# Optimization experiments

Hardware: AMD Instinct MI355X
Metric: run time of the kernel (lower is better)

Reference implementation:

```python
import jax, jax.numpy as jnp
import numpy as np

VAR_NUM = [29, 2, 1, 6, 7, 59, 1, 24, 76, 711, 3, 9, 1]  # sums to 929
TEMP = 0.8
EPS = 1e-20


def setup_inputs() -> dict:
    key = jax.random.key(0)
    ks = jax.random.split(key, 8)
    B, D, H, O = 32768, 128, 1024, 929
    s = lambda n: 1.0 / np.sqrt(n)
    return {
        "x": jax.random.normal(ks[0], (B, D), jnp.float32),
        "W1": jax.random.uniform(ks[1], (D, H), jnp.float32, -s(D), s(D)),
        "b1": jax.random.uniform(ks[2], (H,), jnp.float32, -s(D), s(D)),
        "W2": jax.random.uniform(ks[3], (H, H), jnp.float32, -s(H), s(H)),
        "b2": jax.random.uniform(ks[4], (H,), jnp.float32, -s(H), s(H)),
        "W3": jax.random.uniform(ks[5], (H, O), jnp.float32, -s(H), s(H)),
        "b3": jax.random.uniform(ks[6], (O,), jnp.float32, -s(H), s(H)),
        "u": jax.random.uniform(ks[7], (B, O), jnp.float32),  # U(0,1) gumbel base noise
    }


def reference(x, W1, b1, W2, b2, W3, b3, u):
    h = jax.nn.elu(x @ W1 + b1)          # [B, H]
    h = jax.nn.sigmoid(h @ W2 + b2)      # [B, H]
    logits = h @ W3 + b3                 # [B, 929]
    g = -jnp.log(-jnp.log(u + EPS) + EPS)  # gumbel noise, [B, 929]
    outs = []
    off = 0
    for n in VAR_NUM:  # fixed 13 segments
        seg = logits[:, off:off + n]
        if n == 1:
            outs.append(seg)  # passthrough for continuous columns
        else:
            y = (seg + g[:, off:off + n]) / TEMP
            outs.append(jax.nn.softmax(y, axis=-1))
        off += n
    return jnp.concatenate(outs, axis=1)  # [B, 929]
```

## Files before the change

### kernel.cpp

```cpp
#include <hip/hip_runtime.h>
#include <hip/hip_bf16.h>
#include <stdint.h>

#define GEPS 1e-20f

typedef __bf16 bf16x8 __attribute__((ext_vector_type(8)));
typedef float  f32x4  __attribute__((ext_vector_type(4)));

typedef const __attribute__((address_space(1))) uint32_t* gptr32;
typedef __attribute__((address_space(3))) uint32_t* lptr32;

__device__ __forceinline__ void load_lds16(const void* g, void* l) {
    __builtin_amdgcn_global_load_lds((gptr32)g, (lptr32)l, 16, 0, 0);
}

__device__ __forceinline__ uint16_t f2bf(float v) {
    __hip_bfloat16 b = __float2bfloat16(v);
    return *(uint16_t*)&b;
}
__device__ __forceinline__ float bf2f(uint16_t b) {
    uint32_t u = (uint32_t)b << 16;
    return __builtin_bit_cast(float, u);
}

#define LN2   0.69314718056f
#define LOG2E 1.44269504089f
__device__ __forceinline__ float fast_log(float x) { return __builtin_amdgcn_logf(x) * LN2; }
__device__ __forceinline__ float fast_exp(float x) { return __builtin_amdgcn_exp2f(x * LOG2E); }
__device__ __forceinline__ float fast_exp2(float x) { return __builtin_amdgcn_exp2f(x); }
__device__ __forceinline__ float fast_rcp(float x)  { return __builtin_amdgcn_rcpf(x); }

__device__ __forceinline__ void store_val(uint16_t* C, size_t idx, float v) { C[idx] = f2bf(v); }
__device__ __forceinline__ void store_val(float* C, size_t idx, float v)    { C[idx] = v; }

__global__ void cast_bf16(const float* __restrict__ in, uint16_t* __restrict__ out, int n) {
    int i = (blockIdx.x * blockDim.x + threadIdx.x) * 4;
    if (i < n) {
        float4 v = *(const float4*)(in + i);
        ushort4 o;
        o.x = f2bf(v.x); o.y = f2bf(v.y); o.z = f2bf(v.z); o.w = f2bf(v.w);
        *(ushort4*)(out + i) = o;
    }
}

__global__ void transpose_cast(const float* __restrict__ W, uint16_t* __restrict__ Wt,
                               int K, int N, int Npad) {
    __shared__ float tile[64][65];
    const int k0 = blockIdx.y * 64, n0 = blockIdx.x * 64;
    const int tx = threadIdx.x & 63, ty = threadIdx.x >> 6;
    for (int r = ty; r < 64; r += 4) {
        int n = n0 + tx;
        tile[r][tx] = (n < N) ? W[(size_t)(k0 + r) * N + n] : 0.f;
    }
    __syncthreads();
    for (int r = ty; r < 64; r += 4) {
        Wt[(size_t)(n0 + r) * K + k0 + tx] = f2bf(tile[tx][r]);
    }
}

template<int ACT, typename OutT, bool SNG>
__global__ __launch_bounds__(256)
void gemm_bt(const uint16_t* __restrict__ A, const uint16_t* __restrict__ Bt,
             const float* __restrict__ bias, OutT* __restrict__ C,
             float* __restrict__ sngl,
             int K, int Nout, int ldc) {
    __shared__ __align__(16) uint16_t As[128 * 32];
    __shared__ __align__(16) uint16_t Bs[128 * 32];

    const int t    = threadIdx.x;
    const int wave = t >> 6, lane = t & 63;

    const int nbx = gridDim.x;
    const int bid = blockIdx.y * nbx + blockIdx.x;
    const int xcd = bid & 7;
    const int s   = bid >> 3;
    const int nidx = s % nbx;
    const int midx = xcd * (gridDim.y >> 3) + s / nbx;

    const int m0 = midx * 128, n0 = nidx * 128;
    const int wm = (wave >> 1) * 64, wn = (wave & 1) * 64;
    const int quad = lane >> 4;
    const int qk   = quad * 8;
    const int r15  = lane & 15;

    f32x4 acc[4][4] = {};

    const uint16_t* Ag = A  + (size_t)m0 * K;
    const uint16_t* Bg = Bt + (size_t)n0 * K;

    for (int k0 = 0; k0 < K; k0 += 32) {
        __syncthreads();
        #pragma unroll
        for (int rd = 0; rd < 2; ++rd) {
            int c = t + rd * 256;
            int row = c >> 2, kc = (c & 3) * 8;
            load_lds16(Ag + (size_t)row * K + k0 + kc, &As[c * 8]);
            load_lds16(Bg + (size_t)row * K + k0 + kc, &Bs[c * 8]);
        }
        __syncthreads();

        bf16x8 a[4], b[4];
        #pragma unroll
        for (int i = 0; i < 4; ++i)
            a[i] = *(const bf16x8*)&As[(wm + i * 16 + r15) * 32 + qk];
        #pragma unroll
        for (int i = 0; i < 4; ++i)
            b[i] = *(const bf16x8*)&Bs[(wn + i * 16 + r15) * 32 + qk];

        #pragma unroll
        for (int mi = 0; mi < 4; ++mi)
            #pragma unroll
            for (int ni = 0; ni < 4; ++ni)
                acc[mi][ni] = __builtin_amdgcn_mfma_f32_16x16x32_bf16(
                    a[mi], b[ni], acc[mi][ni], 0, 0, 0);
    }

    #pragma unroll
    for (int ni = 0; ni < 4; ++ni) {
        int col = n0 + wn + ni * 16 + r15;
        if (col < Nout) {
            float bv = bias[col];
            bool is_sng = SNG && (col == 31 || col == 104 || col == 928);
            #pragma unroll
            for (int mi = 0; mi < 4; ++mi) {
                #pragma unroll
                for (int r = 0; r < 4; ++r) {
                    int row = m0 + wm + mi * 16 + quad * 4 + r;
                    float v = acc[mi][ni][r] + bv;
                    if (ACT == 1) v = (v > 0.f) ? v : (fast_exp(v) - 1.f);
                    else if (ACT == 2) v = fast_rcp(1.f + fast_exp(-v));
                    store_val(C, (size_t)row * ldc + col, v);
                    if constexpr (SNG) {
                        if (is_sng) sngl[(size_t)row * 929 + col] = v;
                    }
                }
            }
        }
    }
}

#define BARRIER() asm volatile("s_barrier" ::: "memory")
#define VMW6()    asm volatile("s_waitcnt vmcnt(6)" ::: "memory")
#define VMW8()    asm volatile("s_waitcnt vmcnt(8)" ::: "memory")
#define DRAIN()   asm volatile("s_waitcnt vmcnt(0) lgkmcnt(0)" ::: "memory")
#define PRIO1()   __builtin_amdgcn_s_setprio(1)
#define PRIO0()   __builtin_amdgcn_s_setprio(0)

template<int ACT, typename OutT, bool SNG, int K>
__global__ __launch_bounds__(512, 2)
void gemm256(const uint16_t* __restrict__ A, const uint16_t* __restrict__ Bt,
             const float* __restrict__ bias, OutT* __restrict__ C,
             float* __restrict__ sngl, int Nout, int ldc) {
    constexpr int NT = K / 32;
    constexpr int NI = NT / 4;
    constexpr int KB = K * 2;
    static_assert(NT >= 8 && (NT & (NT - 1)) == 0, "need pow2 >= 8 tiles");
    __shared__ __align__(16) char lds[131072];

    const int t = threadIdx.x;
    const int wave = t >> 6, lane = t & 63;
    const int quad = lane >> 4, r15 = lane & 15;
    const int wm = (wave >> 2) * 128, wn = (wave & 3) * 64;

    const int nbx = gridDim.x;
    const int bid = blockIdx.y * nbx + blockIdx.x;
    const int xcd = bid & 7;
    const int sb  = bid >> 3;
    const int nidx = sb % nbx;
    const int midx = xcd * (gridDim.y >> 3) + sb / nbx;
    const int m0 = midx * 256, n0 = nidx * 256;

    const int scb = ((t & 3) ^ ((t >> 3) & 3)) << 4;
    const char* Asrc = (const char*)A  + (size_t)(m0 + (t >> 2)) * KB + scb;
    const char* Bsrc = (const char*)Bt + (size_t)(n0 + (t >> 2)) * KB + scb;

    const int cbR   = (quad ^ ((r15 >> 1) & 3)) << 4;
    const int aRowB = (wm + r15) * 64;
    const int bRowB = (wn + r15) * 64;

    f32x4 acc[8][4] = {};
    bf16x8 aLo[4], aHi[4], bE[4], bO[4];

    auto stgA = [&](int buf, int tile) {
        const char* s = Asrc + tile * 64;
        load_lds16(s,                    &lds[buf * 32768 + t * 16]);
        load_lds16(s + (size_t)128 * KB, &lds[buf * 32768 + 8192 + t * 16]);
    };
    auto stgB = [&](int buf, int tile) {
        const char* s = Bsrc + tile * 64;
        load_lds16(s,                    &lds[buf * 32768 + 16384 + t * 16]);
        load_lds16(s + (size_t)128 * KB, &lds[buf * 32768 + 24576 + t * 16]);
    };
    auto rdAlo = [&](int buf) {
        #pragma unroll
        for (int i = 0; i < 4; ++i)
            aLo[i] = *(const bf16x8*)&lds[buf * 32768 + aRowB + i * 1024 + cbR];
    };
    auto rdAhi = [&](int buf) {
        #pragma unroll
        for (int i = 0; i < 4; ++i)
            aHi[i] = *(const bf16x8*)&lds[buf * 32768 + aRowB + (4 + i) * 1024 + cbR];
    };
    auto rdB = [&](int buf, bf16x8 (&b)[4]) {
        #pragma unroll
        for (int i = 0; i < 4; ++i)
            b[i] = *(const bf16x8*)&lds[buf * 32768 + 16384 + bRowB + i * 1024 + cbR];
    };
    auto mfma16 = [&](int mlo, bf16x8 (&a)[4], bf16x8 (&b)[4]) {
        #pragma unroll
        for (int mi = 0; mi < 4; ++mi)
            #pragma unroll
            for (int ni = 0; ni < 4; ++ni)
                acc[mlo + mi][ni] = __builtin_amdgcn_mfma_f32_16x16x32_bf16(
                    a[mi], b[ni], acc[mlo + mi][ni], 0, 0, 0);
    };

    stgA(0, 0); stgB(0, 0);
    stgA(1, 1); stgB(1, 1);
    stgA(2, 2); stgB(2, 2);
    VMW8(); BARRIER();
    rdAlo(0); rdB(0, bE);

    #pragma unroll 1
    for (int ki = 0; ki < NI; ++ki) {
        const int T = ki * 4;
        rdAhi(0); stgA(3, (T + 3) & (NT - 1));
        PRIO1(); mfma16(0, aLo, bE); PRIO0();
        VMW6(); BARRIER();
        rdAlo(1); rdB(1, bO); stgB(3, (T + 3) & (NT - 1));
        PRIO1(); mfma16(4, aHi, bE); PRIO0();
        BARRIER();
        rdAhi(1); stgA(0, (T + 4) & (NT - 1));
        PRIO1(); mfma16(0, aLo, bO); PRIO0();
        VMW6(); BARRIER();
        rdAlo(2); rdB(2, bE); stgB(0, (T + 4) & (NT - 1));
        PRIO1(); mfma16(4, aHi, bO); PRIO0();
        BARRIER();
        rdAhi(2); stgA(1, (T + 5) & (NT - 1));
        PRIO1(); mfma16(0, aLo, bE); PRIO0();
        VMW6(); BARRIER();
        rdAlo(3); rdB(3, bO); stgB(1, (T + 5) & (NT - 1));
        PRIO1(); mfma16(4, aHi, bE); PRIO0();
        BARRIER();
        rdAhi(3); stgA(2, (T + 6) & (NT - 1));
        PRIO1(); mfma16(0, aLo, bO); PRIO0();
        VMW6(); BARRIER();
        rdAlo(0); rdB(0, bE); stgB(2, (T + 6) & (NT - 1));
        PRIO1(); mfma16(4, aHi, bO); PRIO0();
        BARRIER();
    }
    DRAIN();
    BARRIER();

    #pragma unroll
    for (int ni = 0; ni < 4; ++ni) {
        const int col = wn + ni * 16 + r15;
        const int gc  = n0 + col;
        const float bv = (gc < Nout) ? bias[gc] : 0.f;
        const bool is_sng = SNG && (gc == 31 || gc == 104 || gc == 928);
        #pragma unroll
        for (int mi = 0; mi < 8; ++mi) {
            #pragma unroll
            for (int r = 0; r < 4; ++r) {
                const int row = wm + mi * 16 + quad * 4 + r;
                float v = acc[mi][ni][r] + bv;
                if (ACT == 1) v = (v > 0.f) ? v : (fast_exp(v) - 1.f);
                else if (ACT == 2) v = fast_rcp(1.f + fast_exp(-v));
                *(uint16_t*)&lds[row * 512 + ((col * 2) ^ ((row & 7) << 4))] = f2bf(v);
                if constexpr (SNG) {
                    if (is_sng) sngl[(size_t)(m0 + row) * 929 + gc] = v;
                }
            }
        }
    }
    asm volatile("s_waitcnt lgkmcnt(0)" ::: "memory");
    BARRIER();

    {
        const int rt = t >> 5;
        const int cc = t & 31;
        #pragma unroll 1
        for (int pass = 0; pass < 16; ++pass) {
            const int row = pass * 16 + rt;
            f32x4 v4 = *(const f32x4*)&lds[row * 512 + ((cc * 16) ^ ((row & 7) << 4))];
            *(f32x4*)&C[(size_t)(m0 + row) * ldc + n0 + cc * 8] = v4;
        }
    }
}

#define NEG_BIG (-1e30f)
#define Y2_LG   1.8033688011f

__device__ __forceinline__ float y2_col(const uint16_t* __restrict__ rlg,
                                        const float* __restrict__ ru, int c) {
    float l2u   = __builtin_amdgcn_logf(ru[c] + GEPS);
    float inner = fmaf(-LN2, l2u, GEPS);
    float l2i   = __builtin_amdgcn_logf(inner);
    return fmaf(Y2_LG, bf2f(rlg[c]), -1.25f * l2i);
}

template<int N, int OFF>
__device__ __forceinline__ void seg_small(const uint16_t* __restrict__ rlg,
                                          const float* __restrict__ ru,
                                          float* __restrict__ rout, int l32) {
    static_assert(N <= 32, "seg_small needs N<=32");
    constexpr int GS = (N <= 2) ? 2 : (N <= 4) ? 4 : (N <= 8) ? 8 : (N <= 16) ? 16 : 32;
    const bool act = l32 < N;
    const int  c   = OFF + l32;
    float y = act ? y2_col(rlg, ru, c) : NEG_BIG;
    float m = y;
    #pragma unroll
    for (int o = 1; o < GS; o <<= 1) m = fmaxf(m, __shfl_xor(m, o, 64));
    float e = act ? fast_exp2(y - m) : 0.f;
    float s = e;
    #pragma unroll
    for (int o = 1; o < GS; o <<= 1) s += __shfl_xor(s, o, 64);
    if (act) rout[c] = e * fast_rcp(s);
}

template<int N, int OFF>
__device__ __forceinline__ void seg_wide(const uint16_t* __restrict__ rlg,
                                         const float* __restrict__ ru,
                                         float* __restrict__ rout, int lane) {
    constexpr int IT = (N + 63) / 64;
    float y[IT];
    float m = NEG_BIG;
    #pragma unroll
    for (int i = 0; i < IT; ++i) {
        const int j = i * 64 + lane;
        y[i] = (j < N) ? y2_col(rlg, ru, OFF + j) : NEG_BIG;
        m = fmaxf(m, y[i]);
    }
    #pragma unroll
    for (int o = 1; o < 64; o <<= 1) m = fmaxf(m, __shfl_xor(m, o, 64));
    float s = 0.f;
    #pragma unroll
    for (int i = 0; i < IT; ++i) {
        float e = fast_exp2(y[i] - m);
        y[i] = e;
        s += e;
    }
    #pragma unroll
    for (int o = 1; o < 64; o <<= 1) s += __shfl_xor(s, o, 64);
    const float inv = fast_rcp(s);
    #pragma unroll
    for (int i = 0; i < IT; ++i) {
        const int j = i * 64 + lane;
        if (j < N) rout[OFF + j] = y[i] * inv;
    }
}

__global__ __launch_bounds__(256)
void gumbel_epilogue(const uint16_t* __restrict__ lg, float* __restrict__ out,
                     const float* __restrict__ u, int B) {
    const int wave = threadIdx.x >> 6, lane = threadIdx.x & 63;
    const int l32  = lane & 31, half = lane >> 5;
    const int rowA = blockIdx.x * 8 + wave * 2;
    if (rowA >= B) return;

    const size_t uoA  = (size_t)rowA * 929;
    const size_t uoB  = uoA + 929;
    const size_t lgoA = (size_t)rowA * 1024;
    const size_t lgoB = lgoA + 1024;
    const size_t uoH  = half ? uoB  : uoA;
    const size_t lgoH = half ? lgoB : lgoA;

    const uint16_t* lgH = lg  + lgoH;
    const float*    uH  = u   + uoH;
    float*          oH  = out + uoH;
    seg_small<29,   0>(lgH, uH, oH, l32);
    seg_small< 2,  29>(lgH, uH, oH, l32);
    seg_small< 6,  32>(lgH, uH, oH, l32);
    seg_small< 7,  38>(lgH, uH, oH, l32);
    seg_small<24, 105>(lgH, uH, oH, l32);
    seg_small< 3, 916>(lgH, uH, oH, l32);
    seg_small< 9, 919>(lgH, uH, oH, l32);

    const uint16_t* lgA = lg + lgoA; const float* uA = u + uoA; float* oA = out + uoA;
    const uint16_t* lgB = lg + lgoB; const float* uB = u + uoB; float* oB = out + uoB;
    seg_wide< 59,  45>(lgA, uA, oA, lane);
    seg_wide< 59,  45>(lgB, uB, oB, lane);
    seg_wide< 76, 129>(lgA, uA, oA, lane);
    seg_wide< 76, 129>(lgB, uB, oB, lane);
    seg_wide<711, 205>(lgA, uA, oA, lane);
    seg_wide<711, 205>(lgB, uB, oB, lane);
}

extern "C" void kernel_launch(void* const* d_in, const int* in_sizes, int n_in,
                              void* d_out, int out_size, void* d_ws, size_t ws_size,
                              hipStream_t stream) {
    const float* x  = (const float*)d_in[0];
    const float* W1 = (const float*)d_in[1];
    const float* b1 = (const float*)d_in[2];
    const float* W2 = (const float*)d_in[3];
    const float* b2 = (const float*)d_in[4];
    const float* W3 = (const float*)d_in[5];
    const float* b3 = (const float*)d_in[6];
    const float* u  = (const float*)d_in[7];
    float* out = (float*)d_out;

    const int B = 32768, D = 128, H = 1024, O = 929, OP = 1024;

    char* ws = (char*)d_ws;
    uint16_t* xb  = (uint16_t*)ws; ws += (size_t)B * D * 2;
    uint16_t* w1t = (uint16_t*)ws; ws += (size_t)H * D * 2;
    uint16_t* w2t = (uint16_t*)ws; ws += (size_t)H * H * 2;
    uint16_t* w3t = (uint16_t*)ws; ws += (size_t)OP * H * 2;
    uint16_t* h1  = (uint16_t*)ws; ws += (size_t)B * H * 2;
    uint16_t* h2  = (uint16_t*)ws; ws += (size_t)B * H * 2;
    uint16_t* lg  = h1;

    cast_bf16<<<(B * D / 4 + 255) / 256, 256, 0, stream>>>(x, xb, B * D);
    transpose_cast<<<dim3(H / 64, D / 64), 256, 0, stream>>>(W1, w1t, D, H, H);
    transpose_cast<<<dim3(H / 64, H / 64), 256, 0, stream>>>(W2, w2t, H, H, H);
    transpose_cast<<<dim3(OP / 64, H / 64), 256, 0, stream>>>(W3, w3t, H, O, OP);

    gemm_bt<1, uint16_t, false><<<dim3(H / 128, B / 128), 256, 0, stream>>>(
        xb, w1t, b1, h1, nullptr, D, H, H);
    gemm256<2, uint16_t, false, 1024><<<dim3(H / 256, B / 256), 512, 0, stream>>>(
        h1, w2t, b2, h2, nullptr, H, H);
    gemm256<0, uint16_t, true, 1024><<<dim3(OP / 256, B / 256), 512, 0, stream>>>(
        h2, w3t, b3, lg, out, O, 1024);

    gumbel_epilogue<<<B / 8, 256, 0, stream>>>(lg, out, u, B);
}
```

Baseline: 465.2 us.

## Use 256-tile pipelined GEMM for layer 1 and batch four rows per wave in epilogue

The first layer (K=128) now runs through the 256x256 pipelined gemm256 kernel instead of the simple 128-tile gemm_bt, with the tile-count assertion relaxed to allow K=128 (NT=4). The Gumbel-softmax epilogue now handles 16 rows per block, and each wave processes the wide segments for four rows at once so their loads and shuffle reductions can overlap. The intent is to cut per-tile overhead in layer 1 and raise memory-level parallelism in the epilogue. Risks are that the pipelined prologue with only 4 K-tiles may not be valid or efficient, and that the epilogue now uses more registers and launches fewer blocks.

```diff
diff --git a/kernel.cpp b/kernel.cpp
--- a/kernel.cpp
+++ b/kernel.cpp
@@ -58,87 +58,6 @@
     }
 }
 
-template<int ACT, typename OutT, bool SNG>
-__global__ __launch_bounds__(256)
-void gemm_bt(const uint16_t* __restrict__ A, const uint16_t* __restrict__ Bt,
-             const float* __restrict__ bias, OutT* __restrict__ C,
-             float* __restrict__ sngl,
-             int K, int Nout, int ldc) {
-    __shared__ __align__(16) uint16_t As[128 * 32];
-    __shared__ __align__(16) uint16_t Bs[128 * 32];
-
-    const int t    = threadIdx.x;
-    const int wave = t >> 6, lane = t & 63;
-
-    const int nbx = gridDim.x;
-    const int bid = blockIdx.y * nbx + blockIdx.x;
-    const int xcd = bid & 7;
-    const int s   = bid >> 3;
-    const int nidx = s % nbx;
-    const int midx = xcd * (gridDim.y >> 3) + s / nbx;
-
-    const int m0 = midx * 128, n0 = nidx * 128;
-    const int wm = (wave >> 1) * 64, wn = (wave & 1) * 64;
-    const int quad = lane >> 4;
-    const int qk   = quad * 8;
-    const int r15  = lane & 15;
-
-    f32x4 acc[4][4] = {};
-
-    const uint16_t* Ag = A  + (size_t)m0 * K;
-    const uint16_t* Bg = Bt + (size_t)n0 * K;
-
-    for (int k0 = 0; k0 < K; k0 += 32) {
-        __syncthreads();
-        #pragma unroll
-        for (int rd = 0; rd < 2; ++rd) {
-            int c = t + rd * 256;
-            int row = c >> 2, kc = (c & 3) * 8;
-            load_lds16(Ag + (size_t)row * K + k0 + kc, &As[c * 8]);
-            load_lds16(Bg + (size_t)row * K + k0 + kc, &Bs[c * 8]);
-        }
-        __syncthreads();
-
-        bf16x8 a[4], b[4];
-        #pragma unroll
-        for (int i = 0; i < 4; ++i)
-            a[i] = *(const bf16x8*)&As[(wm + i * 16 + r15) * 32 + qk];
-        #pragma unroll
-        for (int i = 0; i < 4; ++i)
-            b[i] = *(const bf16x8*)&Bs[(wn + i * 16 + r15) * 32 + qk];
-
-        #pragma unroll
-        for (int mi = 0; mi < 4; ++mi)
-            #pragma unroll
-            for (int ni = 0; ni < 4; ++ni)
-                acc[mi][ni] = __builtin_amdgcn_mfma_f32_16x16x32_bf16(
-                    a[mi], b[ni], acc[mi][ni], 0, 0, 0);
-    }
-
-    #pragma unroll
-    for (int ni = 0; ni < 4; ++ni) {
-        int col = n0 + wn + ni * 16 + r15;
-        if (col < Nout) {
-            float bv = bias[col];
-            bool is_sng = SNG && (col == 31 || col == 104 || col == 928);
-            #pragma unroll
-            for (int mi = 0; mi < 4; ++mi) {
-                #pragma unroll
-                for (int r = 0; r < 4; ++r) {
-                    int row = m0 + wm + mi * 16 + quad * 4 + r;
-                    float v = acc[mi][ni][r] + bv;
-                    if (ACT == 1) v = (v > 0.f) ? v : (fast_exp(v) - 1.f);
-                    else if (ACT == 2) v = fast_rcp(1.f + fast_exp(-v));
-                    store_val(C, (size_t)row * ldc + col, v);
-                    if constexpr (SNG) {
-                        if (is_sng) sngl[(size_t)row * 929 + col] = v;
-                    }
-                }
-            }
-        }
-    }
-}
-
 #define BARRIER() asm volatile("s_barrier" ::: "memory")
 #define VMW6()    asm volatile("s_waitcnt vmcnt(6)" ::: "memory")
 #define VMW8()    asm volatile("s_waitcnt vmcnt(8)" ::: "memory")
@@ -154,7 +73,7 @@
     constexpr int NT = K / 32;
     constexpr int NI = NT / 4;
     constexpr int KB = K * 2;
-    static_assert(NT >= 8 && (NT & (NT - 1)) == 0, "need pow2 >= 8 tiles");
+    static_assert(NT >= 4 && (NT & (NT - 1)) == 0, "need pow2 >= 4 tiles");
     __shared__ __align__(16) char lds[131072];
 
     const int t = threadIdx.x;
@@ -319,34 +238,53 @@
 }
 
 template<int N, int OFF>
-__device__ __forceinline__ void seg_wide(const uint16_t* __restrict__ rlg,
-                                         const float* __restrict__ ru,
-                                         float* __restrict__ rout, int lane) {
+__device__ __forceinline__ void seg_wide4(const uint16_t* __restrict__ lg0,
+                                          const float* __restrict__ u0,
+                                          float* __restrict__ o0, int lane) {
     constexpr int IT = (N + 63) / 64;
-    float y[IT];
-    float m = NEG_BIG;
+    float y[4][IT];
+    float m[4] = {NEG_BIG, NEG_BIG, NEG_BIG, NEG_BIG};
     #pragma unroll
     for (int i = 0; i < IT; ++i) {
         const int j = i * 64 + lane;
-        y[i] = (j < N) ? y2_col(rlg, ru, OFF + j) : NEG_BIG;
-        m = fmaxf(m, y[i]);
-    }
-    #pragma unroll
-    for (int o = 1; o < 64; o <<= 1) m = fmaxf(m, __shfl_xor(m, o, 64));
-    float s = 0.f;
+        #pragma unroll
+        for (int r = 0; r < 4; ++r) {
+            y[r][i] = (j < N) ? y2_col(lg0 + (size_t)r * 1024, u0 + (size_t)r * 929, OFF + j)
+                              : NEG_BIG;
+            m[r] = fmaxf(m[r], y[r][i]);
+        }
+    }
+    #pragma unroll
+    for (int o = 1; o < 64; o <<= 1) {
+        #pragma unroll
+        for (int r = 0; r < 4; ++r) m[r] = fmaxf(m[r], __shfl_xor(m[r], o, 64));
+    }
+    float s[4] = {0.f, 0.f, 0.f, 0.f};
     #pragma unroll
     for (int i = 0; i < IT; ++i) {
-        float e = fast_exp2(y[i] - m);
-        y[i] = e;
-        s += e;
-    }
-    #pragma unroll
-    for (int o = 1; o < 64; o <<= 1) s += __shfl_xor(s, o, 64);
-    const float inv = fast_rcp(s);
+        #pragma unroll
+        for (int r = 0; r < 4; ++r) {
+            float e = fast_exp2(y[r][i] - m[r]);
+            y[r][i] = e;
+            s[r] += e;
+        }
+    }
+    #pragma unroll
+    for (int o = 1; o < 64; o <<= 1) {
+        #pragma unroll
+        for (int r = 0; r < 4; ++r) s[r] += __shfl_xor(s[r], o, 64);
+    }
+    float inv[4];
+    #pragma unroll
+    for (int r = 0; r < 4; ++r) inv[r] = fast_rcp(s[r]);
     #pragma unroll
     for (int i = 0; i < IT; ++i) {
         const int j = i * 64 + lane;
-        if (j < N) rout[OFF + j] = y[i] * inv;
+        if (j < N) {
+            #pragma unroll
+            for (int r = 0; r < 4; ++r)
+                o0[(size_t)r * 929 + OFF + j] = y[r][i] * inv[r];
+        }
     }
 }
 
@@ -355,35 +293,30 @@
                      const float* __restrict__ u, int B) {
     const int wave = threadIdx.x >> 6, lane = threadIdx.x & 63;
     const int l32  = lane & 31, half = lane >> 5;
-    const int rowA = blockIdx.x * 8 + wave * 2;
-    if (rowA >= B) return;
-
-    const size_t uoA  = (size_t)rowA * 929;
-    const size_t uoB  = uoA + 929;
-    const size_t lgoA = (size_t)rowA * 1024;
-    const size_t lgoB = lgoA + 1024;
-    const size_t uoH  = half ? uoB  : uoA;
-    const size_t lgoH = half ? lgoB : lgoA;
-
-    const uint16_t* lgH = lg  + lgoH;
-    const float*    uH  = u   + uoH;
-    float*          oH  = out + uoH;
-    seg_small<29,   0>(lgH, uH, oH, l32);
-    seg_small< 2,  29>(lgH, uH, oH, l32);
-    seg_small< 6,  32>(lgH, uH, oH, l32);
-    seg_small< 7,  38>(lgH, uH, oH, l32);
-    seg_small<24, 105>(lgH, uH, oH, l32);
-    seg_small< 3, 916>(lgH, uH, oH, l32);
-    seg_small< 9, 919>(lgH, uH, oH, l32);
-
-    const uint16_t* lgA = lg + lgoA; const float* uA = u + uoA; float* oA = out + uoA;
-    const uint16_t* lgB = lg + lgoB; const float* uB = u + uoB; float* oB = out + uoB;
-    seg_wide< 59,  45>(lgA, uA, oA, lane);
-    seg_wide< 59,  45>(lgB, uB, oB, lane);
-    seg_wide< 76, 129>(lgA, uA, oA, lane);
-    seg_wide< 76, 129>(lgB, uB, oB, lane);
-    seg_wide<711, 205>(lgA, uA, oA, lane);
-    seg_wide<711, 205>(lgB, uB, oB, lane);
+    const int r0 = blockIdx.x * 16 + wave * 4;
+    if (r0 >= B) return;
+
+    #pragma unroll
+    for (int rr = 0; rr < 2; ++rr) {
+        const int row = r0 + half * 2 + rr;
+        const uint16_t* lgH = lg  + (size_t)row * 1024;
+        const float*    uH  = u   + (size_t)row * 929;
+        float*          oH  = out + (size_t)row * 929;
+        seg_small<29,   0>(lgH, uH, oH, l32);
+        seg_small< 2,  29>(lgH, uH, oH, l32);
+        seg_small< 6,  32>(lgH, uH, oH, l32);
+        seg_small< 7,  38>(lgH, uH, oH, l32);
+        seg_small<24, 105>(lgH, uH, oH, l32);
+        seg_small< 3, 916>(lgH, uH, oH, l32);
+        seg_small< 9, 919>(lgH, uH, oH, l32);
+    }
+
+    const uint16_t* lg0 = lg  + (size_t)r0 * 1024;
+    const float*    u0  = u   + (size_t)r0 * 929;
+    float*          o0  = out + (size_t)r0 * 929;
+    seg_wide4< 59,  45>(lg0, u0, o0, lane);
+    seg_wide4< 76, 129>(lg0, u0, o0, lane);
+    seg_wide4<711, 205>(lg0, u0, o0, lane);
 }
 
 extern "C" void kernel_launch(void* const* d_in, const int* in_sizes, int n_in,
@@ -415,12 +348,12 @@
     transpose_cast<<<dim3(H / 64, H / 64), 256, 0, stream>>>(W2, w2t, H, H, H);
     transpose_cast<<<dim3(OP / 64, H / 64), 256, 0, stream>>>(W3, w3t, H, O, OP);
 
-    gemm_bt<1, uint16_t, false><<<dim3(H / 128, B / 128), 256, 0, stream>>>(
-        xb, w1t, b1, h1, nullptr, D, H, H);
+    gemm256<1, uint16_t, false, 128><<<dim3(H / 256, B / 256), 512, 0, stream>>>(
+        xb, w1t, b1, h1, nullptr, H, H);
     gemm256<2, uint16_t, false, 1024><<<dim3(H / 256, B / 256), 512, 0, stream>>>(
         h1, w2t, b2, h2, nullptr, H, H);
     gemm256<0, uint16_t, true, 1024><<<dim3(OP / 256, B / 256), 512, 0, stream>>>(
         h2, w3t, b3, lg, out, O, 1024);
 
-    gumbel_epilogue<<<B / 8, 256, 0, stream>>>(lg, out, u, B);
-}
+    gumbel_epilogue<<<B / 16, 256, 0, stream>>>(lg, out, u, B);
+}
```

Measured after the change: 483.9 us. 1.04x slower.
